# Performance work log

Measured on AMD Instinct MI355X. Metric: run time of the kernel, lower is better.

The kernel has to match this reference:

```python
import jax, jax.numpy as jnp
import numpy as np

EMBED_DIM = 512
NUM_HEADS = 16
WINDOW = 8
SHIFT = 4
NUM_PATCHES = 64
NEG_INF = -1e9


def _attention_mask():
    # group map over the full patch grid, as in calculate_attention_mask
    P, s, ws = NUM_PATCHES, SHIFT, WINDOW
    g = np.zeros((P, P), dtype=np.float32)
    g[:, -s:] = 1
    g[-s:, :] = 2
    g[-s:, -s:] = 3
    nw = P // ws
    # (h ws a, w ws b) -> (h*w, ws*ws)
    gw = g.reshape(nw, ws, nw, ws).transpose(0, 2, 1, 3).reshape(nw * nw, ws * ws)
    same = gw[:, None, :] == gw[:, :, None]  # column - row == 0 -> allowed
    return jnp.asarray(same)  # (nW, S, S) bool, True = keep


def setup_inputs() -> dict:
    key = jax.random.key(0)
    ks = jax.random.split(key, 5)
    B, P, C = 16, NUM_PATCHES, EMBED_DIM
    sd = 1.0 / np.sqrt(C)
    return {
        "x": jax.random.normal(ks[0], (B, P, P, C), dtype=jnp.float32),
        "w_qkv": jax.random.normal(ks[1], (3 * C, C), dtype=jnp.float32) * sd,
        "b_qkv": jax.random.normal(ks[2], (3 * C,), dtype=jnp.float32) * 0.02,
        "w_out": jax.random.normal(ks[3], (C, C), dtype=jnp.float32) * sd,
        "b_out": jax.random.normal(ks[4], (C,), dtype=jnp.float32) * 0.02,
    }


def reference(x, w_qkv, b_qkv, w_out, b_out):
    B, P, _, C = x.shape
    ws, H = WINDOW, NUM_HEADS
    d = C // H
    nw = P // ws
    S = ws * ws
    scale = d ** (-0.5)

    # shift (roll backwards)
    xs = jnp.roll(x, (-SHIFT, -SHIFT), axis=(1, 2))
    # window partition: (B, nw, ws, nw, ws, C) -> (B*nw*nw, S, C)
    xw = xs.reshape(B, nw, ws, nw, ws, C).transpose(0, 1, 3, 2, 4, 5)
    xw = xw.reshape(B * nw * nw, S, C)

    qkv = xw @ w_qkv.T + b_qkv  # (Bn, S, 3C)
    q, k, v = jnp.split(qkv, 3, axis=-1)
    # head partition: (Bn, S, H, d) -> (Bn, H, S, d)
    part = lambda t: t.reshape(-1, S, H, d).transpose(0, 2, 1, 3)
    q, k, v = part(q), part(k), part(v)

    scores = jnp.einsum('bhqd,bhkd->bhqk', q, k) * scale  # (Bn, H, S, S)

    mask = _attention_mask()  # (nW, S, S) bool
    scores = scores.reshape(B, nw * nw, H, S, S)
    scores = jnp.where(mask[None, :, None], scores, NEG_INF)
    attn = jax.nn.softmax(scores, axis=-1)  # dropout p=0 (inference)
    attn = attn.reshape(B * nw * nw, H, S, S)

    out = jnp.einsum('bhqk,bhkd->bhqd', attn, v)  # (Bn, H, S, d)
    out = out.transpose(0, 2, 1, 3).reshape(B * nw * nw, S, C)  # merge heads
    out = out @ w_out.T + b_out

    # window merge: (B*nw*nw, S, C) -> (B, P, P, C)
    out = out.reshape(B, nw, nw, ws, ws, C).transpose(0, 1, 3, 2, 4, 5)
    out = out.reshape(B, P, P, C)
    # roll forwards
    return jnp.roll(out, (SHIFT, SHIFT), axis=(1, 2))
```

## Files before the change

### kernel.cpp

```cpp
#include <hip/hip_runtime.h>


using f16   = _Float16;
using f16x8 = __attribute__((ext_vector_type(8))) _Float16;
using f16x4 = __attribute__((ext_vector_type(4))) _Float16;
using f32x4 = __attribute__((ext_vector_type(4))) float;

#define MFMA16(a, b, c) __builtin_amdgcn_mfma_f32_16x16x32_f16((a), (b), (c), 0, 0, 0)
#define SCHEDBAR() __builtin_amdgcn_sched_barrier(0)
#define VMCNT0() asm volatile("s_waitcnt vmcnt(0)" ::: "memory")
#define LGKM0()  asm volatile("s_waitcnt lgkmcnt(0)" ::: "memory")
#define BAR()    __builtin_amdgcn_s_barrier()

static constexpr int QK_HALF = 65536 * 512;

__device__ __forceinline__ void nts4f(f32x4 v, float* p) {
  __builtin_nontemporal_store(v, (f32x4*)p);
}

__device__ __forceinline__ int tok2patch(int t) {
  int b = t >> 12, rem = t & 4095;
  int widx = rem >> 6, s = rem & 63;
  int pr = (((widx >> 3) << 3) + (s >> 3) + 4) & 63;
  int pc = (((widx & 7) << 3) + (s & 7) + 4) & 63;
  return ((b << 12) | (pr << 6) | pc) << 9;
}

__device__ __forceinline__ f16x8 cvt8(float4 a, float4 b) {
  f16x8 h = { (f16)a.x, (f16)a.y, (f16)a.z, (f16)a.w,
              (f16)b.x, (f16)b.y, (f16)b.z, (f16)b.w };
  return h;
}

__global__ __launch_bounds__(512, 2) void k_qkv(const float* __restrict__ x,
                                                const float* __restrict__ wq,
                                                const float* __restrict__ bq,
                                                f16* __restrict__ qk,
                                                f16* __restrict__ vt) {
  __shared__ __align__(16) char smem[86016];
  f16* const B0 = (f16*)smem;
  f16* const B1 = (f16*)(smem + 8192);

  const int tid = threadIdx.x;
  const int lane = tid & 63, wave = tid >> 6;
  const int jlo = lane & 15, g = lane >> 4;
  const int bm = blockIdx.x;

  const int nl = tid >> 2, kq = tid & 3;
  const int bslot = (kq ^ ((nl >> 1) & 3)) * 8;

  const int r0 = tok2patch(bm * 256 + wave * 32 + jlo);
  const int r1 = tok2patch(bm * 256 + wave * 32 + 16 + jlo);
  f16x8 af[2][16];
#pragma unroll
  for (int kg = 0; kg < 4; ++kg) {
    float4 t0[4][2], t1[4][2];
#pragma unroll
    for (int k4 = 0; k4 < 4; ++k4) {
      const int ko = (kg * 4 + k4) * 32 + g * 8;
      t0[k4][0] = *(const float4*)(x + r0 + ko);
      t0[k4][1] = *(const float4*)(x + r0 + ko + 4);
      t1[k4][0] = *(const float4*)(x + r1 + ko);
      t1[k4][1] = *(const float4*)(x + r1 + ko + 4);
    }
#pragma unroll
    for (int k4 = 0; k4 < 4; ++k4) {
      af[0][kg * 4 + k4] = cvt8(t0[k4][0], t0[k4][1]);
      af[1][kg * 4 + k4] = cvt8(t1[k4][0], t1[k4][1]);
    }
    SCHEDBAR();
  }

  f32x4 acc[2][8] = {};
  float4 rb[2];
#define LOADB(U2)                                                         \
  do {                                                                    \
    const int bn2_ = (U2) >> 4, k2_ = ((U2) & 15) * 32;                   \
    const float* bs_ = wq + (bn2_ * 128 + nl) * 512 + k2_ + kq * 8;       \
    rb[0] = *(const float4*)(bs_); rb[1] = *(const float4*)(bs_ + 4);     \
  } while (0)
#define WRITEB(Bp) do { *(f16x8*)((Bp) + nl * 32 + bslot) = cvt8(rb[0], rb[1]); } while (0)

  LOADB(0);
  SCHEDBAR();
  VMCNT0();
  WRITEB(B0);
  LOADB(1);
  LGKM0();
  BAR();

#pragma unroll 1
  for (int bn = 0; bn < 12; ++bn) {
    f16* const Cw = (f16*)(smem + 16384 + wave * 8704);
#pragma unroll
    for (int ks = 0; ks < 16; ++ks) {
      const int u = bn * 16 + ks;
      f16* const Bc = (u & 1) ? B1 : B0;
      f16* const Bn = (u & 1) ? B0 : B1;
      f16x8 bf[8];
#pragma unroll
      for (int nt = 0; nt < 8; ++nt) {
        const int n = nt * 16 + jlo;
        bf[nt] = *(const f16x8*)(Bc + n * 32 + ((g ^ ((n >> 1) & 3)) * 8));
      }
      __builtin_amdgcn_s_setprio(1);
#pragma unroll
      for (int mt = 0; mt < 2; ++mt)
#pragma unroll
        for (int nt = 0; nt < 8; ++nt)
          acc[mt][nt] = MFMA16(af[mt][ks], bf[nt], acc[mt][nt]);
      __builtin_amdgcn_s_setprio(0);
      VMCNT0();
      if (u + 1 < 192) WRITEB(Bn);
      SCHEDBAR();
      if (u + 2 < 192) LOADB(u + 2);
      LGKM0();
      BAR();
    }
    float bias[8];
#pragma unroll
    for (int nt = 0; nt < 8; ++nt) bias[nt] = bq[bn * 128 + nt * 16 + jlo];
    if (bn < 8) {
#pragma unroll
      for (int mt = 0; mt < 2; ++mt)
#pragma unroll
        for (int nt = 0; nt < 8; ++nt)
#pragma unroll
          for (int r = 0; r < 4; ++r)
            Cw[(mt * 16 + g * 4 + r) * 136 + nt * 16 + jlo] =
                (f16)(acc[mt][nt][r] + bias[nt]);
      LGKM0();
      f16* const gb = (bn < 4) ? (qk + bn * 128) : (qk + QK_HALF + (bn - 4) * 128);
#pragma unroll
      for (int p = 0; p < 8; ++p) {
        const int lr = (p >> 1) * 8 + (lane >> 3);
        const int ch = (p & 1) * 8 + (lane & 7);
        const int trow = bm * 256 + wave * 32 + lr;
        *(f16x8*)(gb + trow * 512 + ch * 8) = *(const f16x8*)(Cw + lr * 136 + ch * 8);
      }
    } else {
      const int w = (bm * 256 + wave * 32) >> 6;
      const int s0 = (wave * 32) & 63;
#pragma unroll
      for (int hf = 0; hf < 2; ++hf) {
#pragma unroll
        for (int n2 = 0; n2 < 4; ++n2) {
          const int nt = hf * 4 + n2;
#pragma unroll
          for (int mt = 0; mt < 2; ++mt) {
            f16x4 pk = { (f16)(acc[mt][nt][0] + bias[nt]), (f16)(acc[mt][nt][1] + bias[nt]),
                         (f16)(acc[mt][nt][2] + bias[nt]), (f16)(acc[mt][nt][3] + bias[nt]) };
            *(f16x4*)(Cw + (n2 * 16 + jlo) * 48 + mt * 16 + g * 4) = pk;
          }
        }
        LGKM0();
#pragma unroll
        for (int p = 0; p < 4; ++p) {
          const int cl = p * 16 + (lane >> 2);
          const int ch = lane & 3;
          const int n = (bn - 8) * 128 + hf * 64 + cl;
          const int h = n >> 5, d = n & 31;
          *(f16x8*)(vt + ((w * 16 + h) * 32 + d) * 64 + s0 + ch * 8) =
              *(const f16x8*)(Cw + cl * 48 + ch * 8);
        }
      }
    }
#pragma unroll
    for (int mt = 0; mt < 2; ++mt)
#pragma unroll
      for (int nt = 0; nt < 8; ++nt)
        acc[mt][nt] = (f32x4){0.f, 0.f, 0.f, 0.f};
  }
#undef LOADB
#undef WRITEB
}

__global__ __launch_bounds__(256) void k_attn(const f16* __restrict__ qk,
                                              const f16* __restrict__ vt,
                                              f16* __restrict__ ao) {
  __shared__ f16 P[4][64 * 72];
  const int w = blockIdx.x;
  const int widx = w & 63;
  const bool er = (widx >> 3) == 7;
  const bool ec = (widx & 7) == 7;
  const int tid = threadIdx.x;
  const int lane = tid & 63, wave = tid >> 6;
  const int jlo = lane & 15, g = lane >> 4;
  const int tb = w * 64;
  f16* Pw = P[wave];
  const float scale = 0.17677669529663687f;

#pragma unroll 1
  for (int hh = 0; hh < 4; ++hh) {
    const int h = wave * 4 + hh;
    f16x8 qa[4], kb[4];
#pragma unroll
    for (int mt = 0; mt < 4; ++mt)
      qa[mt] = *(const f16x8*)(qk + (tb + mt * 16 + jlo) * 512 + h * 32 + g * 8);
#pragma unroll
    for (int nt = 0; nt < 4; ++nt)
      kb[nt] = *(const f16x8*)(qk + QK_HALF + (tb + nt * 16 + jlo) * 512 + h * 32 + g * 8);
    f32x4 sc[4][4] = {};
#pragma unroll
    for (int mt = 0; mt < 4; ++mt)
#pragma unroll
      for (int nt = 0; nt < 4; ++nt)
        sc[mt][nt] = MFMA16(qa[mt], kb[nt], sc[mt][nt]);

    int gj[4];
#pragma unroll
    for (int nt = 0; nt < 4; ++nt) {
      int j = nt * 16 + jlo;
      gj[nt] = ((er && ((j >> 3) >= 4)) ? 2 : 0) | ((ec && ((j & 7) >= 4)) ? 1 : 0);
    }
    float rinv[4][4];
#pragma unroll
    for (int mt = 0; mt < 4; ++mt) {
#pragma unroll
      for (int r = 0; r < 4; ++r) {
        const int i = mt * 16 + g * 4 + r;
        const int gi = ((er && ((i >> 3) >= 4)) ? 2 : 0) | ((ec && ((i & 7) >= 4)) ? 1 : 0);
        float v0 = (gi == gj[0]) ? sc[mt][0][r] * scale : -1e9f;
        float v1 = (gi == gj[1]) ? sc[mt][1][r] * scale : -1e9f;
        float v2 = (gi == gj[2]) ? sc[mt][2][r] * scale : -1e9f;
        float v3 = (gi == gj[3]) ? sc[mt][3][r] * scale : -1e9f;
        float m = fmaxf(fmaxf(v0, v1), fmaxf(v2, v3));
        m = fmaxf(m, __shfl_xor(m, 1));
        m = fmaxf(m, __shfl_xor(m, 2));
        m = fmaxf(m, __shfl_xor(m, 4));
        m = fmaxf(m, __shfl_xor(m, 8));
        float p0 = __expf(v0 - m), p1 = __expf(v1 - m);
        float p2 = __expf(v2 - m), p3 = __expf(v3 - m);
        float s = p0 + p1 + p2 + p3;
        s += __shfl_xor(s, 1);
        s += __shfl_xor(s, 2);
        s += __shfl_xor(s, 4);
        s += __shfl_xor(s, 8);
        rinv[mt][r] = 1.0f / s;
        sc[mt][0][r] = p0; sc[mt][1][r] = p1; sc[mt][2][r] = p2; sc[mt][3][r] = p3;
      }
    }
#pragma unroll
    for (int mt = 0; mt < 4; ++mt)
#pragma unroll
      for (int nt = 0; nt < 4; ++nt)
#pragma unroll
        for (int r = 0; r < 4; ++r)
          Pw[(mt * 16 + g * 4 + r) * 72 + nt * 16 + jlo] = (f16)sc[mt][nt][r];
    asm volatile("s_waitcnt lgkmcnt(0)" ::: "memory");

    f32x4 o[4][2] = {};
#pragma unroll
    for (int ks = 0; ks < 2; ++ks) {
      f16x8 pa[4], vb[2];
#pragma unroll
      for (int mt = 0; mt < 4; ++mt)
        pa[mt] = *(const f16x8*)((const char*)Pw + (mt * 16 + jlo) * 144 + ks * 64 + g * 16);
#pragma unroll
      for (int nt = 0; nt < 2; ++nt)
        vb[nt] = *(const f16x8*)(vt + ((w * 16 + h) * 32 + nt * 16 + jlo) * 64 + ks * 32 + g * 8);
#pragma unroll
      for (int mt = 0; mt < 4; ++mt)
#pragma unroll
        for (int nt = 0; nt < 2; ++nt)
          o[mt][nt] = MFMA16(pa[mt], vb[nt], o[mt][nt]);
    }
#pragma unroll
    for (int mt = 0; mt < 4; ++mt)
#pragma unroll
      for (int nt = 0; nt < 2; ++nt)
#pragma unroll
        for (int r = 0; r < 4; ++r)
          Pw[(mt * 16 + g * 4 + r) * 40 + nt * 16 + jlo] =
              (f16)(o[mt][nt][r] * rinv[mt][r]);
    f16* arow = ao + (tb + lane) * 512 + h * 32;
#pragma unroll
    for (int c = 0; c < 4; ++c)
      *(f16x8*)(arow + c * 8) = *(const f16x8*)(Pw + lane * 40 + c * 8);
  }
}

__global__ __launch_bounds__(512, 2) void k_out(const f16* __restrict__ ao,
                                                const float* __restrict__ wo,
                                                const float* __restrict__ bo,
                                                float* __restrict__ out) {
  __shared__ __align__(16) char smem[86016];
  f16* const B0 = (f16*)smem;
  f16* const B1 = (f16*)(smem + 8192);

  const int tid = threadIdx.x;
  const int lane = tid & 63, wave = tid >> 6;
  const int jlo = lane & 15, g = lane >> 4;
  const int bm = blockIdx.x;

  const int nl = tid >> 2, kq = tid & 3;
  const int bslot = (kq ^ ((nl >> 1) & 3)) * 8;

  const f16* const a0 = ao + (bm * 256 + wave * 32 + jlo) * 512 + g * 8;
  const f16* const a1 = a0 + 16 * 512;
  f16x8 af[2][16];
#pragma unroll
  for (int ks = 0; ks < 16; ++ks) {
    af[0][ks] = *(const f16x8*)(a0 + ks * 32);
    af[1][ks] = *(const f16x8*)(a1 + ks * 32);
  }

  f32x4 acc[2][8] = {};
  float4 rb[2];
#define LOADB(U2)                                                         \
  do {                                                                    \
    const int bn2_ = (U2) >> 4, k2_ = ((U2) & 15) * 32;                   \
    const float* bs_ = wo + (bn2_ * 128 + nl) * 512 + k2_ + kq * 8;       \
    rb[0] = *(const float4*)(bs_); rb[1] = *(const float4*)(bs_ + 4);     \
  } while (0)
#define WRITEB(Bp) do { *(f16x8*)((Bp) + nl * 32 + bslot) = cvt8(rb[0], rb[1]); } while (0)

  LOADB(0);
  SCHEDBAR();
  VMCNT0();
  WRITEB(B0);
  LOADB(1);
  LGKM0();
  BAR();

#pragma unroll 1
  for (int bn = 0; bn < 4; ++bn) {
    float* const Cw = (float*)(smem + 16384 + wave * 8704);
#pragma unroll
    for (int ks = 0; ks < 16; ++ks) {
      const int u = bn * 16 + ks;
      f16* const Bc = (u & 1) ? B1 : B0;
      f16* const Bn = (u & 1) ? B0 : B1;
      f16x8 bf[8];
#pragma unroll
      for (int nt = 0; nt < 8; ++nt) {
        const int n = nt * 16 + jlo;
        bf[nt] = *(const f16x8*)(Bc + n * 32 + ((g ^ ((n >> 1) & 3)) * 8));
      }
      __builtin_amdgcn_s_setprio(1);
#pragma unroll
      for (int mt = 0; mt < 2; ++mt)
#pragma unroll
        for (int nt = 0; nt < 8; ++nt)
          acc[mt][nt] = MFMA16(af[mt][ks], bf[nt], acc[mt][nt]);
      __builtin_amdgcn_s_setprio(0);
      VMCNT0();
      if (u + 1 < 64) WRITEB(Bn);
      SCHEDBAR();
      if (u + 2 < 64) LOADB(u + 2);
      LGKM0();
      BAR();
    }
#pragma unroll
    for (int hf = 0; hf < 2; ++hf) {
#pragma unroll
      for (int n2 = 0; n2 < 4; ++n2) {
        const int nt = hf * 4 + n2;
        const float bias = bo[bn * 128 + nt * 16 + jlo];
#pragma unroll
        for (int mt = 0; mt < 2; ++mt)
#pragma unroll
          for (int r = 0; r < 4; ++r)
            Cw[(mt * 16 + g * 4 + r) * 68 + n2 * 16 + jlo] = acc[mt][nt][r] + bias;
      }
      LGKM0();
#pragma unroll
      for (int p = 0; p < 8; ++p) {
        const int lr = (p >> 1) * 8 + (lane >> 3);
        const int ch = (p & 1) * 8 + (lane & 7);
        const int trow = bm * 256 + wave * 32 + lr;
        nts4f(*(const f32x4*)(Cw + lr * 68 + ch * 4),
              out + tok2patch(trow) + bn * 128 + hf * 64 + ch * 4);
      }
      LGKM0();
    }
#pragma unroll
    for (int mt = 0; mt < 2; ++mt)
#pragma unroll
      for (int nt = 0; nt < 8; ++nt)
        acc[mt][nt] = (f32x4){0.f, 0.f, 0.f, 0.f};
  }
#undef LOADB
#undef WRITEB
}

extern "C" void kernel_launch(void* const* d_in, const int* in_sizes, int n_in,
                              void* d_out, int out_size, void* d_ws, size_t ws_size,
                              hipStream_t stream) {
  const float* x  = (const float*)d_in[0];
  const float* wq = (const float*)d_in[1];
  const float* bq = (const float*)d_in[2];
  const float* wo = (const float*)d_in[3];
  const float* bo = (const float*)d_in[4];
  float* out = (float*)d_out;

  f16* qk = (f16*)d_out;
  f16* ao = (f16*)d_ws;
  f16* vt = (f16*)((char*)d_ws + (64u << 20));

  k_qkv<<<dim3(256), 512, 0, stream>>>(x, wq, bq, qk, vt);
  k_attn<<<dim3(1024), 256, 0, stream>>>(qk, vt, ao);
  k_out<<<dim3(256), 512, 0, stream>>>(ao, wo, bo, out);
}
```

Measured before the change: 377.4 us.

## Widen weight K-stage to 128 to cut barriers in QKV and output GEMMs

Both projection GEMMs now stage a 128-wide K slice of the weight into double-buffered LDS per barrier instead of a 32-wide slice. Each slice is loaded in two halves that are interleaved with the MFMA sub-steps, and the LDS swizzle changes to an XOR over 8 slots per 128-element row. The goal is four times fewer workgroup barriers and waitcnt stalls per output tile, and longer MFMA runs between synchronisations. In exchange, LDS use grows to about 132 KB per block and more registers hold in-flight weight data, which could limit occupancy or scheduling.

Measured after the change: 425.6 us. +12.8%, slower.

```diff
diff --git a/kernel.cpp b/kernel.cpp
--- a/kernel.cpp
+++ b/kernel.cpp
@@ -37,17 +37,14 @@
                                                 const float* __restrict__ bq,
                                                 f16* __restrict__ qk,
                                                 f16* __restrict__ vt) {
-  __shared__ __align__(16) char smem[86016];
+  __shared__ __align__(16) char smem[135168];
   f16* const B0 = (f16*)smem;
-  f16* const B1 = (f16*)(smem + 8192);
+  f16* const B1 = (f16*)(smem + 32768);
 
   const int tid = threadIdx.x;
   const int lane = tid & 63, wave = tid >> 6;
   const int jlo = lane & 15, g = lane >> 4;
   const int bm = blockIdx.x;
-
-  const int nl = tid >> 2, kq = tid & 3;
-  const int bslot = (kq ^ ((nl >> 1) & 3)) * 8;
 
   const int r0 = tok2patch(bm * 256 + wave * 32 + jlo);
   const int r1 = tok2patch(bm * 256 + wave * 32 + 16 + jlo);
@@ -71,105 +68,138 @@
     SCHEDBAR();
   }
 
+  const int nl = tid >> 2, kq = tid & 3;
+  const int s0w = kq * 2;
   f32x4 acc[2][8] = {};
-  float4 rb[2];
-#define LOADB(U2)                                                         \
-  do {                                                                    \
-    const int bn2_ = (U2) >> 4, k2_ = ((U2) & 15) * 32;                   \
-    const float* bs_ = wq + (bn2_ * 128 + nl) * 512 + k2_ + kq * 8;       \
-    rb[0] = *(const float4*)(bs_); rb[1] = *(const float4*)(bs_ + 4);     \
+  float4 rb[4];
+
+#define LOADB(P, H)                                                          \
+  do {                                                                       \
+    const float* bs_ = wq + (((P) >> 2) * 128 + nl) * 512 +                  \
+                       ((P) & 3) * 128 + (H) * 64 + kq * 16;                 \
+    rb[0] = *(const float4*)(bs_);      rb[1] = *(const float4*)(bs_ + 4);   \
+    rb[2] = *(const float4*)(bs_ + 8);  rb[3] = *(const float4*)(bs_ + 12);  \
   } while (0)
-#define WRITEB(Bp) do { *(f16x8*)((Bp) + nl * 32 + bslot) = cvt8(rb[0], rb[1]); } while (0)
-
-  LOADB(0);
-  SCHEDBAR();
-  VMCNT0();
-  WRITEB(B0);
-  LOADB(1);
+#define WRITEB(Bp, H)                                                        \
+  do {                                                                       \
+    *(f16x8*)((Bp) + nl * 128 + ((((H) * 8 + s0w)     ^ (nl & 7)) * 8)) =    \
+        cvt8(rb[0], rb[1]);                                                  \
+    *(f16x8*)((Bp) + nl * 128 + ((((H) * 8 + s0w + 1) ^ (nl & 7)) * 8)) =    \
+        cvt8(rb[2], rb[3]);                                                  \
+  } while (0)
+
+  LOADB(0, 0); SCHEDBAR(); VMCNT0(); WRITEB(B0, 0);
+  LOADB(0, 1); SCHEDBAR(); VMCNT0(); WRITEB(B0, 1);
+  LOADB(1, 0); SCHEDBAR();
   LGKM0();
   BAR();
 
 #pragma unroll 1
-  for (int bn = 0; bn < 12; ++bn) {
-    f16* const Cw = (f16*)(smem + 16384 + wave * 8704);
-#pragma unroll
-    for (int ks = 0; ks < 16; ++ks) {
-      const int u = bn * 16 + ks;
-      f16* const Bc = (u & 1) ? B1 : B0;
-      f16* const Bn = (u & 1) ? B0 : B1;
-      f16x8 bf[8];
-#pragma unroll
-      for (int nt = 0; nt < 8; ++nt) {
-        const int n = nt * 16 + jlo;
-        bf[nt] = *(const f16x8*)(Bc + n * 32 + ((g ^ ((n >> 1) & 3)) * 8));
-      }
-      __builtin_amdgcn_s_setprio(1);
+  for (int p = 0; p < 48; ++p) {
+    f16* const Bc = (p & 1) ? B1 : B0;
+    f16* const Bn = (p & 1) ? B0 : B1;
+
+#pragma unroll
+    for (int half = 0; half < 2; ++half) {
+#pragma unroll
+      for (int s2 = 0; s2 < 2; ++s2) {
+        const int ks = half * 2 + s2;
+        const int kst = (p & 3) * 4 + ks;
+        f16x8 bf[8];
+#pragma unroll
+        for (int nt = 0; nt < 8; ++nt) {
+          const int n = nt * 16 + jlo;
+          const int slot = (ks * 4 + g) ^ (n & 7);
+          bf[nt] = *(const f16x8*)(Bc + n * 128 + slot * 8);
+        }
+        __builtin_amdgcn_s_setprio(1);
+#pragma unroll
+        for (int mt = 0; mt < 2; ++mt)
+#pragma unroll
+          for (int nt = 0; nt < 8; ++nt)
+            acc[mt][nt] = MFMA16(af[mt][kst], bf[nt], acc[mt][nt]);
+        __builtin_amdgcn_s_setprio(0);
+      }
+      if (half == 0) {
+        if (p < 47) {
+          VMCNT0();
+          WRITEB(Bn, 0);
+          SCHEDBAR();
+          LOADB(p + 1, 1);
+          SCHEDBAR();
+        }
+      } else {
+        if (p < 47) {
+          VMCNT0();
+          WRITEB(Bn, 1);
+          SCHEDBAR();
+          if (p < 46) { LOADB(p + 2, 0); SCHEDBAR(); }
+        }
+        LGKM0();
+        BAR();
+      }
+    }
+
+    if ((p & 3) == 3) {
+      const int bn = p >> 2;
+      float bias[8];
+#pragma unroll
+      for (int nt = 0; nt < 8; ++nt) bias[nt] = bq[bn * 128 + nt * 16 + jlo];
+      if (bn < 8) {
+        f16* const Cw = (f16*)(smem + 65536 + wave * 8704);
+#pragma unroll
+        for (int mt = 0; mt < 2; ++mt)
+#pragma unroll
+          for (int nt = 0; nt < 8; ++nt)
+#pragma unroll
+            for (int r = 0; r < 4; ++r)
+              Cw[(mt * 16 + g * 4 + r) * 136 + nt * 16 + jlo] =
+                  (f16)(acc[mt][nt][r] + bias[nt]);
+        LGKM0();
+        f16* const gb = (bn < 4) ? (qk + bn * 128) : (qk + QK_HALF + (bn - 4) * 128);
+#pragma unroll
+        for (int q = 0; q < 8; ++q) {
+          const int lr = (q >> 1) * 8 + (lane >> 3);
+          const int ch = (q & 1) * 8 + (lane & 7);
+          const int trow = bm * 256 + wave * 32 + lr;
+          *(f16x8*)(gb + trow * 512 + ch * 8) = *(const f16x8*)(Cw + lr * 136 + ch * 8);
+        }
+        LGKM0();
+      } else {
+        f16* const Cw = (f16*)(smem + 65536 + wave * 8704);
+        const int w = bm * 4 + (wave >> 1);
+        const int s0 = (wave * 32) & 63;
+#pragma unroll
+        for (int hf = 0; hf < 2; ++hf) {
+#pragma unroll
+          for (int n2 = 0; n2 < 4; ++n2) {
+            const int nt = hf * 4 + n2;
+#pragma unroll
+            for (int mt = 0; mt < 2; ++mt) {
+              f16x4 pk = { (f16)(acc[mt][nt][0] + bias[nt]), (f16)(acc[mt][nt][1] + bias[nt]),
+                           (f16)(acc[mt][nt][2] + bias[nt]), (f16)(acc[mt][nt][3] + bias[nt]) };
+              *(f16x4*)(Cw + (n2 * 16 + jlo) * 48 + mt * 16 + g * 4) = pk;
+            }
+          }
+          LGKM0();
+#pragma unroll
+          for (int q = 0; q < 4; ++q) {
+            const int cl = q * 16 + (lane >> 2);
+            const int ch = lane & 3;
+            const int n = (bn - 8) * 128 + hf * 64 + cl;
+            const int h = n >> 5, d = n & 31;
+            *(f16x8*)(vt + ((w * 16 + h) * 32 + d) * 64 + s0 + ch * 8) =
+                *(const f16x8*)(Cw + cl * 48 + ch * 8);
+          }
+          LGKM0();
+        }
+      }
 #pragma unroll
       for (int mt = 0; mt < 2; ++mt)
 #pragma unroll
         for (int nt = 0; nt < 8; ++nt)
-          acc[mt][nt] = MFMA16(af[mt][ks], bf[nt], acc[mt][nt]);
-      __builtin_amdgcn_s_setprio(0);
-      VMCNT0();
-      if (u + 1 < 192) WRITEB(Bn);
-      SCHEDBAR();
-      if (u + 2 < 192) LOADB(u + 2);
-      LGKM0();
-      BAR();
-    }
-    float bias[8];
-#pragma unroll
-    for (int nt = 0; nt < 8; ++nt) bias[nt] = bq[bn * 128 + nt * 16 + jlo];
-    if (bn < 8) {
-#pragma unroll
-      for (int mt = 0; mt < 2; ++mt)
-#pragma unroll
-        for (int nt = 0; nt < 8; ++nt)
-#pragma unroll
-          for (int r = 0; r < 4; ++r)
-            Cw[(mt * 16 + g * 4 + r) * 136 + nt * 16 + jlo] =
-                (f16)(acc[mt][nt][r] + bias[nt]);
-      LGKM0();
-      f16* const gb = (bn < 4) ? (qk + bn * 128) : (qk + QK_HALF + (bn - 4) * 128);
-#pragma unroll
-      for (int p = 0; p < 8; ++p) {
-        const int lr = (p >> 1) * 8 + (lane >> 3);
-        const int ch = (p & 1) * 8 + (lane & 7);
-        const int trow = bm * 256 + wave * 32 + lr;
-        *(f16x8*)(gb + trow * 512 + ch * 8) = *(const f16x8*)(Cw + lr * 136 + ch * 8);
-      }
-    } else {
-      const int w = (bm * 256 + wave * 32) >> 6;
-      const int s0 = (wave * 32) & 63;
-#pragma unroll
-      for (int hf = 0; hf < 2; ++hf) {
-#pragma unroll
-        for (int n2 = 0; n2 < 4; ++n2) {
-          const int nt = hf * 4 + n2;
-#pragma unroll
-          for (int mt = 0; mt < 2; ++mt) {
-            f16x4 pk = { (f16)(acc[mt][nt][0] + bias[nt]), (f16)(acc[mt][nt][1] + bias[nt]),
-                         (f16)(acc[mt][nt][2] + bias[nt]), (f16)(acc[mt][nt][3] + bias[nt]) };
-            *(f16x4*)(Cw + (n2 * 16 + jlo) * 48 + mt * 16 + g * 4) = pk;
-          }
-        }
-        LGKM0();
-#pragma unroll
-        for (int p = 0; p < 4; ++p) {
-          const int cl = p * 16 + (lane >> 2);
-          const int ch = lane & 3;
-          const int n = (bn - 8) * 128 + hf * 64 + cl;
-          const int h = n >> 5, d = n & 31;
-          *(f16x8*)(vt + ((w * 16 + h) * 32 + d) * 64 + s0 + ch * 8) =
-              *(const f16x8*)(Cw + cl * 48 + ch * 8);
-        }
-      }
-    }
-#pragma unroll
-    for (int mt = 0; mt < 2; ++mt)
-#pragma unroll
-      for (int nt = 0; nt < 8; ++nt)
-        acc[mt][nt] = (f32x4){0.f, 0.f, 0.f, 0.f};
+          acc[mt][nt] = (f32x4){0.f, 0.f, 0.f, 0.f};
+    }
   }
 #undef LOADB
 #undef WRITEB
@@ -284,18 +314,15 @@
                                                 const float* __restrict__ wo,
                                                 const float* __restrict__ bo,
                                                 float* __restrict__ out) {
-  __shared__ __align__(16) char smem[86016];
+  __shared__ __align__(16) char smem[135168];
   f16* const B0 = (f16*)smem;
-  f16* const B1 = (f16*)(smem + 8192);
+  f16* const B1 = (f16*)(smem + 32768);
 
   const int tid = threadIdx.x;
   const int lane = tid & 63, wave = tid >> 6;
   const int jlo = lane & 15, g = lane >> 4;
   const int bm = blockIdx.x;
 
-  const int nl = tid >> 2, kq = tid & 3;
-  const int bslot = (kq ^ ((nl >> 1) & 3)) * 8;
-
   const f16* const a0 = ao + (bm * 256 + wave * 32 + jlo) * 512 + g * 8;
   const f16* const a1 = a0 + 16 * 512;
   f16x8 af[2][16];
@@ -305,80 +332,110 @@
     af[1][ks] = *(const f16x8*)(a1 + ks * 32);
   }
 
+  const int nl = tid >> 2, kq = tid & 3;
+  const int s0w = kq * 2;
   f32x4 acc[2][8] = {};
-  float4 rb[2];
-#define LOADB(U2)                                                         \
-  do {                                                                    \
-    const int bn2_ = (U2) >> 4, k2_ = ((U2) & 15) * 32;                   \
-    const float* bs_ = wo + (bn2_ * 128 + nl) * 512 + k2_ + kq * 8;       \
-    rb[0] = *(const float4*)(bs_); rb[1] = *(const float4*)(bs_ + 4);     \
+  float4 rb[4];
+
+#define LOADB(P, H)                                                          \
+  do {                                                                       \
+    const float* bs_ = wo + (((P) >> 2) * 128 + nl) * 512 +                  \
+                       ((P) & 3) * 128 + (H) * 64 + kq * 16;                 \
+    rb[0] = *(const float4*)(bs_);      rb[1] = *(const float4*)(bs_ + 4);   \
+    rb[2] = *(const float4*)(bs_ + 8);  rb[3] = *(const float4*)(bs_ + 12);  \
   } while (0)
-#define WRITEB(Bp) do { *(f16x8*)((Bp) + nl * 32 + bslot) = cvt8(rb[0], rb[1]); } while (0)
-
-  LOADB(0);
-  SCHEDBAR();
-  VMCNT0();
-  WRITEB(B0);
-  LOADB(1);
+#define WRITEB(Bp, H)                                                        \
+  do {                                                                       \
+    *(f16x8*)((Bp) + nl * 128 + ((((H) * 8 + s0w)     ^ (nl & 7)) * 8)) =    \
+        cvt8(rb[0], rb[1]);                                                  \
+    *(f16x8*)((Bp) + nl * 128 + ((((H) * 8 + s0w + 1) ^ (nl & 7)) * 8)) =    \
+        cvt8(rb[2], rb[3]);                                                  \
+  } while (0)
+
+  LOADB(0, 0); SCHEDBAR(); VMCNT0(); WRITEB(B0, 0);
+  LOADB(0, 1); SCHEDBAR(); VMCNT0(); WRITEB(B0, 1);
+  LOADB(1, 0); SCHEDBAR();
   LGKM0();
   BAR();
 
 #pragma unroll 1
-  for (int bn = 0; bn < 4; ++bn) {
-    float* const Cw = (float*)(smem + 16384 + wave * 8704);
-#pragma unroll
-    for (int ks = 0; ks < 16; ++ks) {
-      const int u = bn * 16 + ks;
-      f16* const Bc = (u & 1) ? B1 : B0;
-      f16* const Bn = (u & 1) ? B0 : B1;
-      f16x8 bf[8];
-#pragma unroll
-      for (int nt = 0; nt < 8; ++nt) {
-        const int n = nt * 16 + jlo;
-        bf[nt] = *(const f16x8*)(Bc + n * 32 + ((g ^ ((n >> 1) & 3)) * 8));
-      }
-      __builtin_amdgcn_s_setprio(1);
+  for (int p = 0; p < 16; ++p) {
+    f16* const Bc = (p & 1) ? B1 : B0;
+    f16* const Bn = (p & 1) ? B0 : B1;
+
+#pragma unroll
+    for (int half = 0; half < 2; ++half) {
+#pragma unroll
+      for (int s2 = 0; s2 < 2; ++s2) {
+        const int ks = half * 2 + s2;
+        const int kst = (p & 3) * 4 + ks;
+        f16x8 bf[8];
+#pragma unroll
+        for (int nt = 0; nt < 8; ++nt) {
+          const int n = nt * 16 + jlo;
+          const int slot = (ks * 4 + g) ^ (n & 7);
+          bf[nt] = *(const f16x8*)(Bc + n * 128 + slot * 8);
+        }
+        __builtin_amdgcn_s_setprio(1);
+#pragma unroll
+        for (int mt = 0; mt < 2; ++mt)
+#pragma unroll
+          for (int nt = 0; nt < 8; ++nt)
+            acc[mt][nt] = MFMA16(af[mt][kst], bf[nt], acc[mt][nt]);
+        __builtin_amdgcn_s_setprio(0);
+      }
+      if (half == 0) {
+        if (p < 15) {
+          VMCNT0();
+          WRITEB(Bn, 0);
+          SCHEDBAR();
+          LOADB(p + 1, 1);
+          SCHEDBAR();
+        }
+      } else {
+        if (p < 15) {
+          VMCNT0();
+          WRITEB(Bn, 1);
+          SCHEDBAR();
+          if (p < 14) { LOADB(p + 2, 0); SCHEDBAR(); }
+        }
+        LGKM0();
+        BAR();
+      }
+    }
+
+    if ((p & 3) == 3) {
+      const int bn = p >> 2;
+      float* const Cw = (float*)(smem + 65536 + wave * 8704);
+#pragma unroll
+      for (int hf = 0; hf < 2; ++hf) {
+#pragma unroll
+        for (int n2 = 0; n2 < 4; ++n2) {
+          const int nt = hf * 4 + n2;
+          const float bias = bo[bn * 128 + nt * 16 + jlo];
+#pragma unroll
+          for (int mt = 0; mt < 2; ++mt)
+#pragma unroll
+            for (int r = 0; r < 4; ++r)
+              Cw[(mt * 16 + g * 4 + r) * 68 + n2 * 16 + jlo] = acc[mt][nt][r] + bias;
+        }
+        LGKM0();
+#pragma unroll
+        for (int q = 0; q < 8; ++q) {
+          const int lr = (q >> 1) * 8 + (lane >> 3);
+          const int ch = (q & 1) * 8 + (lane & 7);
+          const int trow = bm * 256 + wave * 32 + lr;
+          nts4f(*(const f32x4*)(Cw + lr * 68 + ch * 4),
+                out + tok2patch(trow) + bn * 128 + hf * 64 + ch * 4);
+        }
+        LGKM0();
+      }
 #pragma unroll
       for (int mt = 0; mt < 2; ++mt)
 #pragma unroll
         for (int nt = 0; nt < 8; ++nt)
-          acc[mt][nt] = MFMA16(af[mt][ks], bf[nt], acc[mt][nt]);
-      __builtin_amdgcn_s_setprio(0);
-      VMCNT0();
-      if (u + 1 < 64) WRITEB(Bn);
-      SCHEDBAR();
-      if (u + 2 < 64) LOADB(u + 2);
-      LGKM0();
-      BAR();
-    }
-#pragma unroll
-    for (int hf = 0; hf < 2; ++hf) {
-#pragma unroll
-      for (int n2 = 0; n2 < 4; ++n2) {
-        const int nt = hf * 4 + n2;
-        const float bias = bo[bn * 128 + nt * 16 + jlo];
-#pragma unroll
-        for (int mt = 0; mt < 2; ++mt)
-#pragma unroll
-          for (int r = 0; r < 4; ++r)
-            Cw[(mt * 16 + g * 4 + r) * 68 + n2 * 16 + jlo] = acc[mt][nt][r] + bias;
-      }
-      LGKM0();
-#pragma unroll
-      for (int p = 0; p < 8; ++p) {
-        const int lr = (p >> 1) * 8 + (lane >> 3);
-        const int ch = (p & 1) * 8 + (lane & 7);
-        const int trow = bm * 256 + wave * 32 + lr;
-        nts4f(*(const f32x4*)(Cw + lr * 68 + ch * 4),
-              out + tok2patch(trow) + bn * 128 + hf * 64 + ch * 4);
-      }
-      LGKM0();
-    }
-#pragma unroll
-    for (int mt = 0; mt < 2; ++mt)
-#pragma unroll
-      for (int nt = 0; nt < 8; ++nt)
-        acc[mt][nt] = (f32x4){0.f, 0.f, 0.f, 0.f};
+          acc[mt][nt] = (f32x4){0.f, 0.f, 0.f, 0.f};
+    }
   }
 #undef LOADB
 #undef WRITEB
```

## Fuse QKV projection and windowed attention into one kernel via LDS

Applied to the files above, without the earlier changes.

Merges the QKV GEMM and the attention kernel into a single kernel. Each block computes Q, K and V for its 256 tokens one head pair at a time (64 output columns), keeps them in LDS, and then runs masked softmax attention for the 4 windows × 2 heads right away. This removes the global-memory write and re-read of the full Q/K tensors and the transposed V, and drops one kernel launch. In exchange the GEMM N-tile shrinks to 64 with a reworked swizzled B layout, LDS use rises to about 140 KB per block, and the attention phase is serialized inside the GEMM loop with extra barriers.

Result: slower. 407.4 us (+7.9%).

```diff
diff --git a/kernel.cpp b/kernel.cpp
--- a/kernel.cpp
+++ b/kernel.cpp
@@ -11,8 +11,6 @@
 #define VMCNT0() asm volatile("s_waitcnt vmcnt(0)" ::: "memory")
 #define LGKM0()  asm volatile("s_waitcnt lgkmcnt(0)" ::: "memory")
 #define BAR()    __builtin_amdgcn_s_barrier()
-
-static constexpr int QK_HALF = 65536 * 512;
 
 __device__ __forceinline__ void nts4f(f32x4 v, float* p) {
   __builtin_nontemporal_store(v, (f32x4*)p);
@@ -32,22 +30,21 @@
   return h;
 }
 
-__global__ __launch_bounds__(512, 2) void k_qkv(const float* __restrict__ x,
-                                                const float* __restrict__ wq,
-                                                const float* __restrict__ bq,
-                                                f16* __restrict__ qk,
-                                                f16* __restrict__ vt) {
-  __shared__ __align__(16) char smem[86016];
-  f16* const B0 = (f16*)smem;
-  f16* const B1 = (f16*)(smem + 8192);
+__global__ __launch_bounds__(512, 2) void k_fused(const float* __restrict__ x,
+                                                  const float* __restrict__ wq,
+                                                  const float* __restrict__ bq,
+                                                  f16* __restrict__ ao) {
+  __shared__ __align__(16) char smem[143360];
+  f16* const Q  = (f16*)smem;
+  f16* const Kl = (f16*)(smem + 36864);
+  f16* const V  = (f16*)(smem + 73728);
+  f16* const B0 = (f16*)(smem + 110592);
+  f16* const B1 = (f16*)(smem + 126976);
 
   const int tid = threadIdx.x;
   const int lane = tid & 63, wave = tid >> 6;
   const int jlo = lane & 15, g = lane >> 4;
   const int bm = blockIdx.x;
-
-  const int nl = tid >> 2, kq = tid & 3;
-  const int bslot = (kq ^ ((nl >> 1) & 3)) * 8;
 
   const int r0 = tok2patch(bm * 256 + wave * 32 + jlo);
   const int r1 = tok2patch(bm * 256 + wave * 32 + 16 + jlo);
@@ -71,213 +68,204 @@
     SCHEDBAR();
   }
 
-  f32x4 acc[2][8] = {};
-  float4 rb[2];
-#define LOADB(U2)                                                         \
-  do {                                                                    \
-    const int bn2_ = (U2) >> 4, k2_ = ((U2) & 15) * 32;                   \
-    const float* bs_ = wq + (bn2_ * 128 + nl) * 512 + k2_ + kq * 8;       \
-    rb[0] = *(const float4*)(bs_); rb[1] = *(const float4*)(bs_ + 4);     \
+  const int nl = tid >> 3, kq = tid & 7;
+  float4 rb[4];
+#define LOADB(P)                                                             \
+  do {                                                                       \
+    const int hg_ = (P) / 12, rem_ = (P) % 12;                               \
+    const int t_ = rem_ >> 2, per_ = rem_ & 3;                               \
+    const float* bs_ = wq + (t_ * 512 + hg_ * 64 + nl) * 512 +               \
+                       per_ * 128 + kq * 16;                                 \
+    rb[0] = *(const float4*)(bs_);      rb[1] = *(const float4*)(bs_ + 4);   \
+    rb[2] = *(const float4*)(bs_ + 8);  rb[3] = *(const float4*)(bs_ + 12);  \
   } while (0)
-#define WRITEB(Bp) do { *(f16x8*)((Bp) + nl * 32 + bslot) = cvt8(rb[0], rb[1]); } while (0)
-
-  LOADB(0);
-  SCHEDBAR();
-  VMCNT0();
-  WRITEB(B0);
-  LOADB(1);
-  LGKM0();
-  BAR();
+#define WRITEB(Bp)                                                           \
+  do {                                                                       \
+    *(f16x8*)((Bp) + nl * 128 + (((kq * 2)     ^ (nl & 7)) * 8)) =           \
+        cvt8(rb[0], rb[1]);                                                  \
+    *(f16x8*)((Bp) + nl * 128 + (((kq * 2 + 1) ^ (nl & 7)) * 8)) =           \
+        cvt8(rb[2], rb[3]);                                                  \
+  } while (0)
+
+  f32x4 acc[2][4] = {};
+  const float scale = 0.17677669529663687f;
+
+  LOADB(0); SCHEDBAR(); VMCNT0(); WRITEB(B0); LOADB(1); SCHEDBAR();
+  LGKM0(); BAR();
 
 #pragma unroll 1
-  for (int bn = 0; bn < 12; ++bn) {
-    f16* const Cw = (f16*)(smem + 16384 + wave * 8704);
-#pragma unroll
-    for (int ks = 0; ks < 16; ++ks) {
-      const int u = bn * 16 + ks;
-      f16* const Bc = (u & 1) ? B1 : B0;
-      f16* const Bn = (u & 1) ? B0 : B1;
-      f16x8 bf[8];
-#pragma unroll
-      for (int nt = 0; nt < 8; ++nt) {
+  for (int p = 0; p < 96; ++p) {
+    f16* const Bc = (p & 1) ? B1 : B0;
+    f16* const Bn = (p & 1) ? B0 : B1;
+
+#pragma unroll
+    for (int ks = 0; ks < 4; ++ks) {
+      const int kst = (p & 3) * 4 + ks;
+      f16x8 bf[4];
+#pragma unroll
+      for (int nt = 0; nt < 4; ++nt) {
         const int n = nt * 16 + jlo;
-        bf[nt] = *(const f16x8*)(Bc + n * 32 + ((g ^ ((n >> 1) & 3)) * 8));
+        bf[nt] = *(const f16x8*)(Bc + n * 128 + (((ks * 4 + g) ^ (n & 7)) * 8));
       }
       __builtin_amdgcn_s_setprio(1);
 #pragma unroll
       for (int mt = 0; mt < 2; ++mt)
 #pragma unroll
-        for (int nt = 0; nt < 8; ++nt)
-          acc[mt][nt] = MFMA16(af[mt][ks], bf[nt], acc[mt][nt]);
+        for (int nt = 0; nt < 4; ++nt)
+          acc[mt][nt] = MFMA16(af[mt][kst], bf[nt], acc[mt][nt]);
       __builtin_amdgcn_s_setprio(0);
+    }
+    if (p + 1 < 96) {
       VMCNT0();
-      if (u + 1 < 192) WRITEB(Bn);
+      WRITEB(Bn);
       SCHEDBAR();
-      if (u + 2 < 192) LOADB(u + 2);
-      LGKM0();
-      BAR();
-    }
-    float bias[8];
-#pragma unroll
-    for (int nt = 0; nt < 8; ++nt) bias[nt] = bq[bn * 128 + nt * 16 + jlo];
-    if (bn < 8) {
-#pragma unroll
-      for (int mt = 0; mt < 2; ++mt)
-#pragma unroll
-        for (int nt = 0; nt < 8; ++nt)
-#pragma unroll
-          for (int r = 0; r < 4; ++r)
-            Cw[(mt * 16 + g * 4 + r) * 136 + nt * 16 + jlo] =
-                (f16)(acc[mt][nt][r] + bias[nt]);
-      LGKM0();
-      f16* const gb = (bn < 4) ? (qk + bn * 128) : (qk + QK_HALF + (bn - 4) * 128);
-#pragma unroll
-      for (int p = 0; p < 8; ++p) {
-        const int lr = (p >> 1) * 8 + (lane >> 3);
-        const int ch = (p & 1) * 8 + (lane & 7);
-        const int trow = bm * 256 + wave * 32 + lr;
-        *(f16x8*)(gb + trow * 512 + ch * 8) = *(const f16x8*)(Cw + lr * 136 + ch * 8);
-      }
-    } else {
-      const int w = (bm * 256 + wave * 32) >> 6;
-      const int s0 = (wave * 32) & 63;
-#pragma unroll
-      for (int hf = 0; hf < 2; ++hf) {
-#pragma unroll
-        for (int n2 = 0; n2 < 4; ++n2) {
-          const int nt = hf * 4 + n2;
-#pragma unroll
-          for (int mt = 0; mt < 2; ++mt) {
+      if (p + 2 < 96) LOADB(p + 2);
+      SCHEDBAR();
+    }
+    LGKM0();
+    BAR();
+
+    if ((p & 3) == 3) {
+      const int hg = p / 12, t = (p % 12) >> 2;
+      float bias[4];
+#pragma unroll
+      for (int nt = 0; nt < 4; ++nt) bias[nt] = bq[t * 512 + hg * 64 + nt * 16 + jlo];
+      if (t < 2) {
+        f16* const dst = (t == 0) ? Q : Kl;
+#pragma unroll
+        for (int mt = 0; mt < 2; ++mt)
+#pragma unroll
+          for (int nt = 0; nt < 4; ++nt)
+#pragma unroll
+            for (int r = 0; r < 4; ++r)
+              dst[(wave * 32 + mt * 16 + g * 4 + r) * 72 + nt * 16 + jlo] =
+                  (f16)(acc[mt][nt][r] + bias[nt]);
+      } else {
+#pragma unroll
+        for (int mt = 0; mt < 2; ++mt)
+#pragma unroll
+          for (int nt = 0; nt < 4; ++nt) {
+            const int rowb = wave * 32 + mt * 16 + g * 4;
+            const int win = rowb >> 6, s0 = rowb & 63;
+            const int col = nt * 16 + jlo, hh = col >> 5, d = col & 31;
             f16x4 pk = { (f16)(acc[mt][nt][0] + bias[nt]), (f16)(acc[mt][nt][1] + bias[nt]),
                          (f16)(acc[mt][nt][2] + bias[nt]), (f16)(acc[mt][nt][3] + bias[nt]) };
-            *(f16x4*)(Cw + (n2 * 16 + jlo) * 48 + mt * 16 + g * 4) = pk;
+            *(f16x4*)(V + ((win * 2 + hh) * 32 + d) * 72 + s0) = pk;
+          }
+      }
+#pragma unroll
+      for (int mt = 0; mt < 2; ++mt)
+#pragma unroll
+        for (int nt = 0; nt < 4; ++nt)
+          acc[mt][nt] = (f32x4){0.f, 0.f, 0.f, 0.f};
+    }
+
+    if (p % 12 == 11) {
+      const int hg = p / 12;
+      const int win = wave >> 1, hh = wave & 1, head = hg * 2 + hh;
+      const int widx = (bm * 4 + win) & 63;
+      const bool er = (widx >> 3) == 7;
+      const bool ec = (widx & 7) == 7;
+      f16* const Pw = (f16*)smem + wave * 4608;
+
+      f16x8 qa[4], kb[4];
+#pragma unroll
+      for (int mt = 0; mt < 4; ++mt)
+        qa[mt] = *(const f16x8*)(Q + (win * 64 + mt * 16 + jlo) * 72 + hh * 32 + g * 8);
+#pragma unroll
+      for (int nt = 0; nt < 4; ++nt)
+        kb[nt] = *(const f16x8*)(Kl + (win * 64 + nt * 16 + jlo) * 72 + hh * 32 + g * 8);
+      int gj[4];
+#pragma unroll
+      for (int nt = 0; nt < 4; ++nt) {
+        int j = nt * 16 + jlo;
+        gj[nt] = ((er && ((j >> 3) >= 4)) ? 2 : 0) | ((ec && ((j & 7) >= 4)) ? 1 : 0);
+      }
+      LGKM0();
+      BAR();
+
+#pragma unroll
+      for (int hf = 0; hf < 2; ++hf) {
+        f32x4 sc[2][4] = {};
+#pragma unroll
+        for (int m2 = 0; m2 < 2; ++m2)
+#pragma unroll
+          for (int nt = 0; nt < 4; ++nt)
+            sc[m2][nt] = MFMA16(qa[hf * 2 + m2], kb[nt], sc[m2][nt]);
+        float rinv[2][4];
+#pragma unroll
+        for (int m2 = 0; m2 < 2; ++m2) {
+#pragma unroll
+          for (int r = 0; r < 4; ++r) {
+            const int i = hf * 32 + m2 * 16 + g * 4 + r;
+            const int gi = ((er && ((i >> 3) >= 4)) ? 2 : 0) | ((ec && ((i & 7) >= 4)) ? 1 : 0);
+            float v0 = (gi == gj[0]) ? sc[m2][0][r] * scale : -1e9f;
+            float v1 = (gi == gj[1]) ? sc[m2][1][r] * scale : -1e9f;
+            float v2 = (gi == gj[2]) ? sc[m2][2][r] * scale : -1e9f;
+            float v3 = (gi == gj[3]) ? sc[m2][3][r] * scale : -1e9f;
+            float m = fmaxf(fmaxf(v0, v1), fmaxf(v2, v3));
+            m = fmaxf(m, __shfl_xor(m, 1));
+            m = fmaxf(m, __shfl_xor(m, 2));
+            m = fmaxf(m, __shfl_xor(m, 4));
+            m = fmaxf(m, __shfl_xor(m, 8));
+            float p0 = __expf(v0 - m), p1 = __expf(v1 - m);
+            float p2 = __expf(v2 - m), p3 = __expf(v3 - m);
+            float s = p0 + p1 + p2 + p3;
+            s += __shfl_xor(s, 1);
+            s += __shfl_xor(s, 2);
+            s += __shfl_xor(s, 4);
+            s += __shfl_xor(s, 8);
+            rinv[m2][r] = 1.0f / s;
+            sc[m2][0][r] = p0; sc[m2][1][r] = p1; sc[m2][2][r] = p2; sc[m2][3][r] = p3;
           }
         }
+#pragma unroll
+        for (int m2 = 0; m2 < 2; ++m2)
+#pragma unroll
+          for (int nt = 0; nt < 4; ++nt)
+#pragma unroll
+            for (int r = 0; r < 4; ++r)
+              Pw[(hf * 32 + m2 * 16 + g * 4 + r) * 72 + nt * 16 + jlo] =
+                  (f16)sc[m2][nt][r];
         LGKM0();
-#pragma unroll
-        for (int p = 0; p < 4; ++p) {
-          const int cl = p * 16 + (lane >> 2);
-          const int ch = lane & 3;
-          const int n = (bn - 8) * 128 + hf * 64 + cl;
-          const int h = n >> 5, d = n & 31;
-          *(f16x8*)(vt + ((w * 16 + h) * 32 + d) * 64 + s0 + ch * 8) =
-              *(const f16x8*)(Cw + cl * 48 + ch * 8);
+
+        f32x4 o[2][2] = {};
+#pragma unroll
+        for (int ks = 0; ks < 2; ++ks) {
+          f16x8 pa[2], vb[2];
+#pragma unroll
+          for (int m2 = 0; m2 < 2; ++m2)
+            pa[m2] = *(const f16x8*)(Pw + (hf * 32 + m2 * 16 + jlo) * 72 + ks * 32 + g * 8);
+#pragma unroll
+          for (int nt = 0; nt < 2; ++nt)
+            vb[nt] = *(const f16x8*)(V + ((win * 2 + hh) * 32 + nt * 16 + jlo) * 72 +
+                                     ks * 32 + g * 8);
+#pragma unroll
+          for (int m2 = 0; m2 < 2; ++m2)
+#pragma unroll
+            for (int nt = 0; nt < 2; ++nt)
+              o[m2][nt] = MFMA16(pa[m2], vb[nt], o[m2][nt]);
         }
-      }
-    }
-#pragma unroll
-    for (int mt = 0; mt < 2; ++mt)
-#pragma unroll
-      for (int nt = 0; nt < 8; ++nt)
-        acc[mt][nt] = (f32x4){0.f, 0.f, 0.f, 0.f};
+#pragma unroll
+        for (int m2 = 0; m2 < 2; ++m2)
+#pragma unroll
+          for (int nt = 0; nt < 2; ++nt)
+#pragma unroll
+            for (int r = 0; r < 4; ++r)
+              Pw[(hf * 32 + m2 * 16 + g * 4 + r) * 40 + nt * 16 + jlo] =
+                  (f16)(o[m2][nt][r] * rinv[m2][r]);
+        LGKM0();
+      }
+      f16* const arow = ao + (bm * 256 + win * 64 + lane) * 512 + head * 32;
+#pragma unroll
+      for (int c = 0; c < 4; ++c)
+        *(f16x8*)(arow + c * 8) = *(const f16x8*)(Pw + lane * 40 + c * 8);
+      LGKM0();
+      BAR();
+    }
   }
 #undef LOADB
 #undef WRITEB
-}
-
-__global__ __launch_bounds__(256) void k_attn(const f16* __restrict__ qk,
-                                              const f16* __restrict__ vt,
-                                              f16* __restrict__ ao) {
-  __shared__ f16 P[4][64 * 72];
-  const int w = blockIdx.x;
-  const int widx = w & 63;
-  const bool er = (widx >> 3) == 7;
-  const bool ec = (widx & 7) == 7;
-  const int tid = threadIdx.x;
-  const int lane = tid & 63, wave = tid >> 6;
-  const int jlo = lane & 15, g = lane >> 4;
-  const int tb = w * 64;
-  f16* Pw = P[wave];
-  const float scale = 0.17677669529663687f;
-
-#pragma unroll 1
-  for (int hh = 0; hh < 4; ++hh) {
-    const int h = wave * 4 + hh;
-    f16x8 qa[4], kb[4];
-#pragma unroll
-    for (int mt = 0; mt < 4; ++mt)
-      qa[mt] = *(const f16x8*)(qk + (tb + mt * 16 + jlo) * 512 + h * 32 + g * 8);
-#pragma unroll
-    for (int nt = 0; nt < 4; ++nt)
-      kb[nt] = *(const f16x8*)(qk + QK_HALF + (tb + nt * 16 + jlo) * 512 + h * 32 + g * 8);
-    f32x4 sc[4][4] = {};
-#pragma unroll
-    for (int mt = 0; mt < 4; ++mt)
-#pragma unroll
-      for (int nt = 0; nt < 4; ++nt)
-        sc[mt][nt] = MFMA16(qa[mt], kb[nt], sc[mt][nt]);
-
-    int gj[4];
-#pragma unroll
-    for (int nt = 0; nt < 4; ++nt) {
-      int j = nt * 16 + jlo;
-      gj[nt] = ((er && ((j >> 3) >= 4)) ? 2 : 0) | ((ec && ((j & 7) >= 4)) ? 1 : 0);
-    }
-    float rinv[4][4];
-#pragma unroll
-    for (int mt = 0; mt < 4; ++mt) {
-#pragma unroll
-      for (int r = 0; r < 4; ++r) {
-        const int i = mt * 16 + g * 4 + r;
-        const int gi = ((er && ((i >> 3) >= 4)) ? 2 : 0) | ((ec && ((i & 7) >= 4)) ? 1 : 0);
-        float v0 = (gi == gj[0]) ? sc[mt][0][r] * scale : -1e9f;
-        float v1 = (gi == gj[1]) ? sc[mt][1][r] * scale : -1e9f;
-        float v2 = (gi == gj[2]) ? sc[mt][2][r] * scale : -1e9f;
-        float v3 = (gi == gj[3]) ? sc[mt][3][r] * scale : -1e9f;
-        float m = fmaxf(fmaxf(v0, v1), fmaxf(v2, v3));
-        m = fmaxf(m, __shfl_xor(m, 1));
-        m = fmaxf(m, __shfl_xor(m, 2));
-        m = fmaxf(m, __shfl_xor(m, 4));
-        m = fmaxf(m, __shfl_xor(m, 8));
-        float p0 = __expf(v0 - m), p1 = __expf(v1 - m);
-        float p2 = __expf(v2 - m), p3 = __expf(v3 - m);
-        float s = p0 + p1 + p2 + p3;
-        s += __shfl_xor(s, 1);
-        s += __shfl_xor(s, 2);
-        s += __shfl_xor(s, 4);
-        s += __shfl_xor(s, 8);
-        rinv[mt][r] = 1.0f / s;
-        sc[mt][0][r] = p0; sc[mt][1][r] = p1; sc[mt][2][r] = p2; sc[mt][3][r] = p3;
-      }
-    }
-#pragma unroll
-    for (int mt = 0; mt < 4; ++mt)
-#pragma unroll
-      for (int nt = 0; nt < 4; ++nt)
-#pragma unroll
-        for (int r = 0; r < 4; ++r)
-          Pw[(mt * 16 + g * 4 + r) * 72 + nt * 16 + jlo] = (f16)sc[mt][nt][r];
-    asm volatile("s_waitcnt lgkmcnt(0)" ::: "memory");
-
-    f32x4 o[4][2] = {};
-#pragma unroll
-    for (int ks = 0; ks < 2; ++ks) {
-      f16x8 pa[4], vb[2];
-#pragma unroll
-      for (int mt = 0; mt < 4; ++mt)
-        pa[mt] = *(const f16x8*)((const char*)Pw + (mt * 16 + jlo) * 144 + ks * 64 + g * 16);
-#pragma unroll
-      for (int nt = 0; nt < 2; ++nt)
-        vb[nt] = *(const f16x8*)(vt + ((w * 16 + h) * 32 + nt * 16 + jlo) * 64 + ks * 32 + g * 8);
-#pragma unroll
-      for (int mt = 0; mt < 4; ++mt)
-#pragma unroll
-        for (int nt = 0; nt < 2; ++nt)
-          o[mt][nt] = MFMA16(pa[mt], vb[nt], o[mt][nt]);
-    }
-#pragma unroll
-    for (int mt = 0; mt < 4; ++mt)
-#pragma unroll
-      for (int nt = 0; nt < 2; ++nt)
-#pragma unroll
-        for (int r = 0; r < 4; ++r)
-          Pw[(mt * 16 + g * 4 + r) * 40 + nt * 16 + jlo] =
-              (f16)(o[mt][nt][r] * rinv[mt][r]);
-    f16* arow = ao + (tb + lane) * 512 + h * 32;
-#pragma unroll
-    for (int c = 0; c < 4; ++c)
-      *(f16x8*)(arow + c * 8) = *(const f16x8*)(Pw + lane * 40 + c * 8);
-  }
 }
 
 __global__ __launch_bounds__(512, 2) void k_out(const f16* __restrict__ ao,
@@ -365,9 +353,9 @@
       }
       LGKM0();
 #pragma unroll
-      for (int p = 0; p < 8; ++p) {
-        const int lr = (p >> 1) * 8 + (lane >> 3);
-        const int ch = (p & 1) * 8 + (lane & 7);
+      for (int q = 0; q < 8; ++q) {
+        const int lr = (q >> 1) * 8 + (lane >> 3);
+        const int ch = (q & 1) * 8 + (lane & 7);
         const int trow = bm * 256 + wave * 32 + lr;
         nts4f(*(const f32x4*)(Cw + lr * 68 + ch * 4),
               out + tok2patch(trow) + bn * 128 + hf * 64 + ch * 4);
@@ -394,11 +382,8 @@
   const float* bo = (const float*)d_in[4];
   float* out = (float*)d_out;
 
-  f16* qk = (f16*)d_out;
   f16* ao = (f16*)d_ws;
-  f16* vt = (f16*)((char*)d_ws + (64u << 20));
-
-  k_qkv<<<dim3(256), 512, 0, stream>>>(x, wq, bq, qk, vt);
-  k_attn<<<dim3(1024), 256, 0, stream>>>(qk, vt, ao);
+
+  k_fused<<<dim3(256), 512, 0, stream>>>(x, wq, bq, ao);
   k_out<<<dim3(256), 512, 0, stream>>>(ao, wo, bo, out);
 }
```
